# Performance work log

Hardware: AMD Instinct MI355X
Metric: run time of the kernel (lower is better)

## Reference

```python
import jax, jax.numpy as jnp
import numpy as np

B, T, D_IN, H, OUT = 512, 512, 64, 256, 64
EPS = 1e-5


def _ln(x, w, b):
    m = x.mean(-1, keepdims=True)
    v = ((x - m) ** 2).mean(-1, keepdims=True)
    return (x - m) / jnp.sqrt(v + EPS) * w + b


def _cell(x, h_prev, Wg, bg, gnw, gnb, Wc, bc, cnw, cnb):
    # LayerNormGRU cell
    combined = jnp.concatenate([x, h_prev], axis=-1)          # [B, D+H]
    rz = _ln(combined @ Wg.T + bg, gnw, gnb)                  # [B, 2H]
    r, z = jnp.split(rz, 2, axis=-1)
    r, z = jax.nn.sigmoid(r), jax.nn.sigmoid(z)
    combined_r = jnp.concatenate([x, r * h_prev], axis=-1)
    n = jnp.tanh(_ln(combined_r @ Wc.T + bc, cnw, cnb))       # [B, H]
    return (1.0 - z) * h_prev + z * n


def setup_inputs() -> dict:
    key = jax.random.key(0)
    ks = jax.random.split(key, 24)

    def uni(k, shape, fan_in):
        lim = 1.0 / np.sqrt(fan_in)
        return jax.random.uniform(k, shape, jnp.float32, -lim, lim)

    d0 = D_IN + H   # layer 0 cell input width
    d1 = H + H      # layer 1 cell input width
    return {
        "x": jax.random.normal(ks[0], (B, T, D_IN), jnp.float32),
        # layer 0
        "Wg0": uni(ks[1], (2 * H, d0), d0), "bg0": uni(ks[2], (2 * H,), d0),
        "gnw0": jnp.ones((2 * H,), jnp.float32), "gnb0": jnp.zeros((2 * H,), jnp.float32),
        "Wc0": uni(ks[3], (H, d0), d0), "bc0": uni(ks[4], (H,), d0),
        "cnw0": jnp.ones((H,), jnp.float32), "cnb0": jnp.zeros((H,), jnp.float32),
        # layer 1
        "Wg1": uni(ks[5], (2 * H, d1), d1), "bg1": uni(ks[6], (2 * H,), d1),
        "gnw1": jnp.ones((2 * H,), jnp.float32), "gnb1": jnp.zeros((2 * H,), jnp.float32),
        "Wc1": uni(ks[7], (H, d1), d1), "bc1": uni(ks[8], (H,), d1),
        "cnw1": jnp.ones((H,), jnp.float32), "cnb1": jnp.zeros((H,), jnp.float32),
        # output head
        "fcW": uni(ks[9], (OUT, H), H), "fcb": uni(ks[10], (OUT,), H),
    }


def reference(x, Wg0, bg0, gnw0, gnb0, Wc0, bc0, cnw0, cnb0,
              Wg1, bg1, gnw1, gnb1, Wc1, bc1, cnw1, cnb1, fcW, fcb):
    b = x.shape[0]
    h_init = (jnp.zeros((b, H), x.dtype), jnp.zeros((b, H), x.dtype))

    def step(carry, xt):
        h0, h1 = carry
        h0 = _cell(xt, h0, Wg0, bg0, gnw0, gnb0, Wc0, bc0, cnw0, cnb0)
        h1 = _cell(h0, h1, Wg1, bg1, gnw1, gnb1, Wc1, bc1, cnw1, cnb1)
        return (h0, h1), None

    (h0, h1), _ = jax.lax.scan(step, h_init, jnp.swapaxes(x, 0, 1))  # scan over T
    return h1 @ fcW.T + fcb  # [B, OUT]
```

## Files before the change

kernel.cpp:

```cpp
#include <hip/hip_runtime.h>


#define B_   512
#define T_   512
#define DIN  64
#define H_   256
#define OUT_ 64
#define EPS_ 1e-5f

typedef __attribute__((ext_vector_type(8))) short bf16x8;
typedef __attribute__((ext_vector_type(4))) float f32x4;

__device__ __forceinline__ unsigned short f2bf(float f) {
  unsigned int u = __float_as_uint(f);
  u += 0x7fffu + ((u >> 16) & 1u);
  return (unsigned short)(u >> 16);
}
__device__ __forceinline__ float bfh(unsigned short u) {
  return __uint_as_float(((unsigned int)u) << 16);
}
__device__ __forceinline__ float sigm_(float x) {
  return __builtin_amdgcn_rcpf(1.f + __expf(-x));
}
__device__ __forceinline__ float tanh_(float x) {
  return 1.f - 2.f * __builtin_amdgcn_rcpf(__expf(2.f * x) + 1.f);
}
template<int C>
__device__ __forceinline__ float dpp_add(float v) {
  int r = __builtin_amdgcn_update_dpp(0, __float_as_int(v), C, 0xF, 0xF, false);
  return v + __int_as_float(r);
}
__device__ __forceinline__ float red16(float v) {
  v = dpp_add<0x121>(v);
  v = dpp_add<0x122>(v);
  v = dpp_add<0x124>(v);
  v = dpp_add<0x128>(v);
  return v;
}

#define PIN8A(a) asm volatile("" : "+a"(a[0]), "+a"(a[1]), "+a"(a[2]), "+a"(a[3]), \
                                   "+a"(a[4]), "+a"(a[5]), "+a"(a[6]), "+a"(a[7]))

__global__ void prep_frag(const float* __restrict__ w, unsigned short* __restrict__ dst,
                          int N, int Ksrc, int koff) {
  int gid = blockIdx.x * 256 + threadIdx.x;
  if (gid >= N * 256) return;
  int n = gid >> 8, k = gid & 255;
  int idx = (((n >> 4) * 8 + (k >> 5)) * 64 + ((n & 15) + 16 * ((k >> 3) & 3))) * 8 + (k & 7);
  dst[idx] = f2bf(w[(size_t)n * Ksrc + koff + k]);
}

__global__ void prep_wx(const float* __restrict__ wg, const float* __restrict__ wc,
                        unsigned short* __restrict__ dst, int KX, int Kg, int Kc) {
  int gid = blockIdx.x * 256 + threadIdx.x;
  if (gid >= 768 * KX) return;
  int n = gid / KX, k = gid - n * KX;
  float v = (n < 512) ? wg[(size_t)n * Kg + k] : wc[(size_t)(n - 512) * Kc + k];
  dst[gid] = f2bf(v);
}

__global__ void bias_cat(const float* __restrict__ bg, const float* __restrict__ bc,
                         float* __restrict__ dst) {
  int i = blockIdx.x * 256 + threadIdx.x;
  if (i < 768) dst[i] = (i < 512) ? bg[i] : bc[i - 512];
}

__device__ __forceinline__ void precomp_tile(
    const void* __restrict__ Asrc, const unsigned short* __restrict__ wx,
    const float* __restrict__ bias, unsigned short* __restrict__ Pc,
    int TC, int t0, int KX, int AFP32,
    int mi, int nb, unsigned short* A_s, unsigned short* B_s, int t256)
{
  const int lane = t256 & 63, wv = t256 >> 6;
  const int m0 = mi * 128;
  const int bt = m0 / (TC * 16);
  const int tt0 = (m0 - bt * TC * 16) >> 4;
  const int mq = wv >> 1, nq = wv & 1;
  const int crow0 = (lane >> 4) * 4;

  f32x4 acc[4][4];
#pragma unroll
  for (int i = 0; i < 4; ++i)
#pragma unroll
    for (int j = 0; j < 4; ++j) acc[i][j] = (f32x4){0, 0, 0, 0};

  for (int kb = 0; kb < (KX >> 6); ++kb) {
    __syncthreads();
#pragma unroll
    for (int it = 0; it < 4; ++it) {
      int s = t256 + it * 256;
      int rg = s >> 3, k8 = s & 7;
      int mt = rg >> 4, r15 = rg & 15;
      int dl = r15 + 16 * (k8 & 3), kc = k8 >> 2;
      if (AFP32) {
        const float* xp = (const float*)Asrc +
            (((size_t)(bt * 16 + r15)) * T_ + (t0 + tt0 + mt)) * DIN + kb * 64 + k8 * 8;
        float4 u0 = *(const float4*)xp, u1 = *(const float4*)(xp + 4);
        unsigned short tmp[8];
        tmp[0] = f2bf(u0.x); tmp[1] = f2bf(u0.y); tmp[2] = f2bf(u0.z); tmp[3] = f2bf(u0.w);
        tmp[4] = f2bf(u1.x); tmp[5] = f2bf(u1.y); tmp[6] = f2bf(u1.z); tmp[7] = f2bf(u1.w);
        *reinterpret_cast<bf16x8*>(&A_s[((mt * 2 + kc) * 64 + dl) * 8]) =
            *reinterpret_cast<bf16x8*>(tmp);
      } else {
        const unsigned short* ap = (const unsigned short*)Asrc +
            ((size_t)(m0 + rg)) * KX + kb * 64 + k8 * 8;
        *reinterpret_cast<bf16x8*>(&A_s[((mt * 2 + kc) * 64 + dl) * 8]) =
            *reinterpret_cast<const bf16x8*>(ap);
      }
      const unsigned short* bp = wx + ((size_t)(nb + rg)) * KX + kb * 64 + k8 * 8;
      *reinterpret_cast<bf16x8*>(&B_s[((mt * 2 + kc) * 64 + dl) * 8]) =
          *reinterpret_cast<const bf16x8*>(bp);
    }
    __syncthreads();
#pragma unroll
    for (int kc = 0; kc < 2; ++kc) {
      bf16x8 av[4], bv[4];
#pragma unroll
      for (int i = 0; i < 4; ++i) {
        av[i] = *reinterpret_cast<const bf16x8*>(&A_s[(((mq * 4 + i) * 2 + kc) * 64 + lane) * 8]);
        bv[i] = *reinterpret_cast<const bf16x8*>(&B_s[(((nq * 4 + i) * 2 + kc) * 64 + lane) * 8]);
      }
#pragma unroll
      for (int i = 0; i < 4; ++i)
#pragma unroll
        for (int j = 0; j < 4; ++j)
          acc[i][j] = __builtin_amdgcn_mfma_f32_16x16x32_bf16(av[i], bv[j], acc[i][j], 0, 0, 0);
    }
  }
  float bb[4];
#pragma unroll
  for (int j = 0; j < 4; ++j) bb[j] = bias[nb + nq * 64 + j * 16 + (lane & 15)];
#pragma unroll
  for (int i = 0; i < 4; ++i) {
    int tt = tt0 + mq * 4 + i;
#pragma unroll
    for (int j = 0; j < 4; ++j) {
      int n = nb + nq * 64 + j * 16 + (lane & 15);
      ushort4 o;
      o.x = f2bf(acc[i][j][0] + bb[j]); o.y = f2bf(acc[i][j][1] + bb[j]);
      o.z = f2bf(acc[i][j][2] + bb[j]); o.w = f2bf(acc[i][j][3] + bb[j]);
      *reinterpret_cast<ushort4*>(&Pc[((size_t)(bt * TC + tt) * 768 + n) * 16 + crow0]) = o;
    }
  }
}

__launch_bounds__(256)
__global__ void precomp_std(const void* __restrict__ Asrc,
                            const unsigned short* __restrict__ wx,
                            const float* __restrict__ bias,
                            unsigned short* __restrict__ Pc,
                            int TC, int t0, int KX, int AFP32) {
  __shared__ __align__(16) unsigned short A_s[8192];
  __shared__ __align__(16) unsigned short B_s[8192];
  precomp_tile(Asrc, wx, bias, Pc, TC, t0, KX, AFP32,
               blockIdx.x, blockIdx.y * 128, A_s, B_s, threadIdx.x);
}

__device__ __forceinline__ void gru_body(
    unsigned char* smem, int bt,
    const unsigned short* __restrict__ gfrag,
    const unsigned short* __restrict__ cfrag,
    const unsigned short* __restrict__ Pc,
    const float* __restrict__ gnw, const float* __restrict__ gnb,
    const float* __restrict__ cnw, const float* __restrict__ cnb,
    float* __restrict__ hstate, unsigned short* __restrict__ h0out,
    int TC, int first)
{
  unsigned short* wc_s = (unsigned short*)smem;
  unsigned short (*h_s)[264]  = (unsigned short(*)[264])(smem + 131072);
  unsigned short (*rh_s)[264] = (unsigned short(*)[264])(smem + 139520);
  float (*sumP)[20] = (float(*)[20])(smem + 147968);
  float (*sqP)[20]  = (float(*)[20])(smem + 148608);

  const int tid = threadIdx.x, lane = tid & 63, wv = tid >> 6;
  const int b0 = bt * 16;
  const int arow = lane & 15, koff = (lane >> 4) * 8, crow0 = (lane >> 4) * 4;
  const int colr0 = 32 * wv + (lane & 15), colr1 = colr0 + 16;
  const int nt0 = 2 * wv, nt1 = 2 * wv + 1, nt2 = 16 + 2 * wv, nt3 = 17 + 2 * wv;

  for (int i = tid; i < 8192; i += 512)
    *reinterpret_cast<bf16x8*>(&wc_s[i * 8]) = *reinterpret_cast<const bf16x8*>(&cfrag[i * 8]);

  bf16x8 wgr0[8], wgr1[8], wgr2[8], wgr3[8];
#pragma unroll
  for (int kc = 0; kc < 8; ++kc) {
    wgr0[kc] = *reinterpret_cast<const bf16x8*>(&gfrag[((nt0 * 8 + kc) * 64 + lane) * 8]);
    wgr1[kc] = *reinterpret_cast<const bf16x8*>(&gfrag[((nt1 * 8 + kc) * 64 + lane) * 8]);
    wgr2[kc] = *reinterpret_cast<const bf16x8*>(&gfrag[((nt2 * 8 + kc) * 64 + lane) * 8]);
    wgr3[kc] = *reinterpret_cast<const bf16x8*>(&gfrag[((nt3 * 8 + kc) * 64 + lane) * 8]);
  }

  const float gw_r0 = gnw[colr0], gb_r0 = gnb[colr0];
  const float gw_r1 = gnw[colr1], gb_r1 = gnb[colr1];
  const float gw_z0 = gnw[256 + colr0], gb_z0 = gnb[256 + colr0];
  const float gw_z1 = gnw[256 + colr1], gb_z1 = gnb[256 + colr1];
  const float cw0 = cnw[colr0], cb0 = cnb[colr0];
  const float cw1 = cnw[colr1], cb1 = cnb[colr1];

  float hm[2][4];
  if (first) {
#pragma unroll
    for (int g = 0; g < 4; ++g) { hm[0][g] = 0.f; hm[1][g] = 0.f; }
    for (int i = tid; i < 16 * 264; i += 512) (&h_s[0][0])[i] = 0;
  } else {
#pragma unroll
    for (int g = 0; g < 4; ++g) {
      hm[0][g] = hstate[(size_t)(b0 + crow0 + g) * 256 + colr0];
      hm[1][g] = hstate[(size_t)(b0 + crow0 + g) * 256 + colr1];
    }
    int r = tid >> 5, c8 = (tid & 31) * 8;
    float4 v0 = *reinterpret_cast<const float4*>(&hstate[(size_t)(b0 + r) * 256 + c8]);
    float4 v1 = *reinterpret_cast<const float4*>(&hstate[(size_t)(b0 + r) * 256 + c8 + 4]);
    ushort4 o0, o1;
    o0.x = f2bf(v0.x); o0.y = f2bf(v0.y); o0.z = f2bf(v0.z); o0.w = f2bf(v0.w);
    o1.x = f2bf(v1.x); o1.y = f2bf(v1.y); o1.z = f2bf(v1.z); o1.w = f2bf(v1.w);
    *reinterpret_cast<ushort4*>(&h_s[r][c8]) = o0;
    *reinterpret_cast<ushort4*>(&h_s[r][c8 + 4]) = o1;
  }
  __syncthreads();

  const unsigned short* Pr = Pc + ((size_t)bt * TC * 768 + colr0) * 16;
  ushort4 npr0 = *reinterpret_cast<const ushort4*>(Pr + crow0);
  ushort4 npr1 = *reinterpret_cast<const ushort4*>(Pr + 256 + crow0);
  ushort4 npz0 = *reinterpret_cast<const ushort4*>(Pr + 4096 + crow0);
  ushort4 npz1 = *reinterpret_cast<const ushort4*>(Pr + 4352 + crow0);
  ushort4 npn0 = *reinterpret_cast<const ushort4*>(Pr + 8192 + crow0);
  ushort4 npn1 = *reinterpret_cast<const ushort4*>(Pr + 8448 + crow0);

  for (int tt = 0; tt < TC; ++tt) {
    PIN8A(wgr0); PIN8A(wgr1); PIN8A(wgr2); PIN8A(wgr3);

    ushort4 pr0 = npr0, pr1 = npr1, pz0 = npz0, pz1 = npz1, pn0 = npn0, pn1 = npn1;
    if (tt + 1 < TC) {
      Pr += 12288;
      npr0 = *reinterpret_cast<const ushort4*>(Pr + crow0);
      npr1 = *reinterpret_cast<const ushort4*>(Pr + 256 + crow0);
      npz0 = *reinterpret_cast<const ushort4*>(Pr + 4096 + crow0);
      npz1 = *reinterpret_cast<const ushort4*>(Pr + 4352 + crow0);
      npn0 = *reinterpret_cast<const ushort4*>(Pr + 8192 + crow0);
      npn1 = *reinterpret_cast<const ushort4*>(Pr + 8448 + crow0);
    }

    f32x4 a0 = {0, 0, 0, 0}, a1 = {0, 0, 0, 0}, a2 = {0, 0, 0, 0}, a3 = {0, 0, 0, 0};
#pragma unroll
    for (int kc = 0; kc < 8; ++kc) {
      bf16x8 av = *reinterpret_cast<const bf16x8*>(&h_s[arow][kc * 32 + koff]);
      a0 = __builtin_amdgcn_mfma_f32_16x16x32_bf16(av, wgr0[kc], a0, 0, 0, 0);
      a1 = __builtin_amdgcn_mfma_f32_16x16x32_bf16(av, wgr1[kc], a1, 0, 0, 0);
      a2 = __builtin_amdgcn_mfma_f32_16x16x32_bf16(av, wgr2[kc], a2, 0, 0, 0);
      a3 = __builtin_amdgcn_mfma_f32_16x16x32_bf16(av, wgr3[kc], a3, 0, 0, 0);
    }
    float vr0[4], vr1[4], vz0[4], vz1[4];
    {
      float s4[4], q4[4];
#pragma unroll
      for (int g = 0; g < 4; ++g) {
        vr0[g] = a0[g] + bfh(((const unsigned short*)&pr0)[g]);
        vr1[g] = a1[g] + bfh(((const unsigned short*)&pr1)[g]);
        vz0[g] = a2[g] + bfh(((const unsigned short*)&pz0)[g]);
        vz1[g] = a3[g] + bfh(((const unsigned short*)&pz1)[g]);
        s4[g] = red16(vr0[g] + vr1[g] + vz0[g] + vz1[g]);
        q4[g] = red16(vr0[g] * vr0[g] + vr1[g] * vr1[g] + vz0[g] * vz0[g] + vz1[g] * vz1[g]);
      }
      if ((lane & 15) == 0) {
        *reinterpret_cast<f32x4*>(&sumP[wv][crow0]) = (f32x4){s4[0], s4[1], s4[2], s4[3]};
        *reinterpret_cast<f32x4*>(&sqP[wv][crow0])  = (f32x4){q4[0], q4[1], q4[2], q4[3]};
      }
    }
    __syncthreads();

    float zf[2][4];
    {
      int sg = lane >> 4, rr = lane & 15;
      float S = sumP[2 * sg][rr] + sumP[2 * sg + 1][rr];
      float Q = sqP[2 * sg][rr] + sqP[2 * sg + 1][rr];
      S += __shfl_xor(S, 16, 64); Q += __shfl_xor(Q, 16, 64);
      S += __shfl_xor(S, 32, 64); Q += __shfl_xor(Q, 32, 64);
      float mn = S * (1.f / 512.f);
      float rs = __builtin_amdgcn_rsqf(Q * (1.f / 512.f) - mn * mn + EPS_);
#pragma unroll
      for (int g = 0; g < 4; ++g) {
        float m_ = __shfl(mn, crow0 + g, 64);
        float r_ = __shfl(rs, crow0 + g, 64);
        float rv0 = sigm_(fmaf((vr0[g] - m_) * r_, gw_r0, gb_r0));
        float rv1 = sigm_(fmaf((vr1[g] - m_) * r_, gw_r1, gb_r1));
        zf[0][g]  = sigm_(fmaf((vz0[g] - m_) * r_, gw_z0, gb_z0));
        zf[1][g]  = sigm_(fmaf((vz1[g] - m_) * r_, gw_z1, gb_z1));
        rh_s[crow0 + g][colr0] = f2bf(rv0 * hm[0][g]);
        rh_s[crow0 + g][colr1] = f2bf(rv1 * hm[1][g]);
      }
    }
    __syncthreads();

    f32x4 c0a = {0, 0, 0, 0}, c1a = {0, 0, 0, 0};
#pragma unroll
    for (int kc = 0; kc < 8; ++kc) {
      bf16x8 av = *reinterpret_cast<const bf16x8*>(&rh_s[arow][kc * 32 + koff]);
      bf16x8 b0v = *reinterpret_cast<const bf16x8*>(&wc_s[((nt0 * 8 + kc) * 64 + lane) * 8]);
      bf16x8 b1v = *reinterpret_cast<const bf16x8*>(&wc_s[((nt1 * 8 + kc) * 64 + lane) * 8]);
      c0a = __builtin_amdgcn_mfma_f32_16x16x32_bf16(av, b0v, c0a, 0, 0, 0);
      c1a = __builtin_amdgcn_mfma_f32_16x16x32_bf16(av, b1v, c1a, 0, 0, 0);
    }
    float vc0[4], vc1[4];
    {
      float s4[4], q4[4];
#pragma unroll
      for (int g = 0; g < 4; ++g) {
        vc0[g] = c0a[g] + bfh(((const unsigned short*)&pn0)[g]);
        vc1[g] = c1a[g] + bfh(((const unsigned short*)&pn1)[g]);
        s4[g] = red16(vc0[g] + vc1[g]);
        q4[g] = red16(vc0[g] * vc0[g] + vc1[g] * vc1[g]);
      }
      if ((lane & 15) == 0) {
        *reinterpret_cast<f32x4*>(&sumP[wv][crow0]) = (f32x4){s4[0], s4[1], s4[2], s4[3]};
        *reinterpret_cast<f32x4*>(&sqP[wv][crow0])  = (f32x4){q4[0], q4[1], q4[2], q4[3]};
      }
    }
    __syncthreads();

    {
      int sg = lane >> 4, rr = lane & 15;
      float S = sumP[2 * sg][rr] + sumP[2 * sg + 1][rr];
      float Q = sqP[2 * sg][rr] + sqP[2 * sg + 1][rr];
      S += __shfl_xor(S, 16, 64); Q += __shfl_xor(Q, 16, 64);
      S += __shfl_xor(S, 32, 64); Q += __shfl_xor(Q, 32, 64);
      float mn = S * (1.f / 256.f);
      float rs = __builtin_amdgcn_rsqf(Q * (1.f / 256.f) - mn * mn + EPS_);
      unsigned short* hrow = h0out ? (h0out + (size_t)(bt * TC + tt) * 4096) : (unsigned short*)nullptr;
#pragma unroll
      for (int g = 0; g < 4; ++g) {
        float m_ = __shfl(mn, crow0 + g, 64);
        float r_ = __shfl(rs, crow0 + g, 64);
        float n0 = tanh_(fmaf((vc0[g] - m_) * r_, cw0, cb0));
        float n1 = tanh_(fmaf((vc1[g] - m_) * r_, cw1, cb1));
        float h0n = fmaf(zf[0][g], n0 - hm[0][g], hm[0][g]);
        float h1n = fmaf(zf[1][g], n1 - hm[1][g], hm[1][g]);
        hm[0][g] = h0n; hm[1][g] = h1n;
        unsigned short hb0 = f2bf(h0n), hb1 = f2bf(h1n);
        h_s[crow0 + g][colr0] = hb0;
        h_s[crow0 + g][colr1] = hb1;
        if (hrow) {
          hrow[(size_t)(crow0 + g) * 256 + colr0] = hb0;
          hrow[(size_t)(crow0 + g) * 256 + colr1] = hb1;
        }
      }
    }
    __syncthreads();
  }

#pragma unroll
  for (int g = 0; g < 4; ++g) {
    hstate[(size_t)(b0 + crow0 + g) * 256 + colr0] = hm[0][g];
    hstate[(size_t)(b0 + crow0 + g) * 256 + colr1] = hm[1][g];
  }
}

__launch_bounds__(512, 2)
__global__ void mega(
    const float* __restrict__ x,
    const unsigned short* __restrict__ g0h, const unsigned short* __restrict__ c0h,
    const unsigned short* __restrict__ g1h, const unsigned short* __restrict__ c1h,
    const unsigned short* __restrict__ wx0, const unsigned short* __restrict__ wx1,
    const float* __restrict__ b768_0, const float* __restrict__ b768_1,
    const float* __restrict__ gnw0, const float* __restrict__ gnb0,
    const float* __restrict__ cnw0, const float* __restrict__ cnb0,
    const float* __restrict__ gnw1, const float* __restrict__ gnb1,
    const float* __restrict__ cnw1, const float* __restrict__ cnb1,
    float* __restrict__ hst0, float* __restrict__ hst1,
    unsigned short* __restrict__ P0a, unsigned short* __restrict__ P0b,
    unsigned short* __restrict__ P1a, unsigned short* __restrict__ P1b,
    unsigned short* __restrict__ h0a, unsigned short* __restrict__ h0b,
    int k, int TC, int NC)
{
  __shared__ __align__(16) unsigned char smem[149504];
  const int bid = blockIdx.x;

  if (bid < 32) {
    if (k >= NC) return;
    unsigned short* P0 = (k & 1) ? P0b : P0a;
    unsigned short* h0 = (k & 1) ? h0b : h0a;
    gru_body(smem, bid, g0h, c0h, P0, gnw0, gnb0, cnw0, cnb0, hst0, h0, TC, k == 0);
  } else if (bid < 64) {
    int kD = k - 2;
    if (kD < 0 || kD >= NC) return;
    unsigned short* P1 = (kD & 1) ? P1b : P1a;
    gru_body(smem, bid - 32, g1h, c1h, P1, gnw1, gnb1, cnw1, cnb1, hst1,
             (unsigned short*)nullptr, TC, kD == 0);
  } else if (bid < 160) {
    int kA = k + 1;
    if (kA >= NC) return;
    unsigned short* P0 = (kA & 1) ? P0b : P0a;
    int team = (bid - 64) * 2 + (threadIdx.x >> 8);
    int t256 = threadIdx.x & 255;
    unsigned short* A_s = (unsigned short*)(smem + (threadIdx.x >> 8) * 32768);
    unsigned short* B_s = A_s + 8192;
    int ntile = 24 * TC;
    for (int i = team; i < ntile; i += 192) {
      int mi = i % (4 * TC), ni = i / (4 * TC);
      precomp_tile(x, wx0, b768_0, P0, TC, kA * TC, 64, 1, mi, ni * 128, A_s, B_s, t256);
    }
  } else {
    int kC = k - 1;
    if (kC < 0 || kC >= NC) return;
    const unsigned short* h0 = (kC & 1) ? h0b : h0a;
    unsigned short* P1 = (kC & 1) ? P1b : P1a;
    int team = (bid - 160) * 2 + (threadIdx.x >> 8);
    int t256 = threadIdx.x & 255;
    unsigned short* A_s = (unsigned short*)(smem + (threadIdx.x >> 8) * 32768);
    unsigned short* B_s = A_s + 8192;
    int ntile = 24 * TC;
    for (int i = team; i < ntile; i += 192) {
      int mi = i % (4 * TC), ni = i / (4 * TC);
      precomp_tile(h0, wx1, b768_1, P1, TC, 0, 256, 0, mi, ni * 128, A_s, B_s, t256);
    }
  }
}

__launch_bounds__(256)
__global__ void head_k(const float* __restrict__ h1, const float* __restrict__ fcW,
                       const float* __restrict__ fcb, float* __restrict__ out) {
  __shared__ float hs[16][256];
  const int tid = threadIdx.x, b0 = blockIdx.x * 16;
  for (int i = tid; i < 16 * 64; i += 256) {
    int r = i >> 6, c4 = (i & 63) * 4;
    *reinterpret_cast<float4*>(&hs[r][c4]) =
        *reinterpret_cast<const float4*>(&h1[(size_t)(b0 + r) * 256 + c4]);
  }
  __syncthreads();
  int r = tid >> 4, o = (tid & 15) * 4;
  float a0 = fcb[o], a1 = fcb[o + 1], a2 = fcb[o + 2], a3 = fcb[o + 3];
  for (int k = 0; k < 256; ++k) {
    float h = hs[r][k];
    a0 = fmaf(h, fcW[(size_t)(o + 0) * 256 + k], a0);
    a1 = fmaf(h, fcW[(size_t)(o + 1) * 256 + k], a1);
    a2 = fmaf(h, fcW[(size_t)(o + 2) * 256 + k], a2);
    a3 = fmaf(h, fcW[(size_t)(o + 3) * 256 + k], a3);
  }
  float4 ov = {a0, a1, a2, a3};
  *reinterpret_cast<float4*>(&out[(size_t)(b0 + r) * 64 + o]) = ov;
}

extern "C" void kernel_launch(void* const* d_in, const int* in_sizes, int n_in,
                              void* d_out, int out_size, void* d_ws, size_t ws_size,
                              hipStream_t stream) {
  (void)in_sizes; (void)n_in; (void)out_size;
  const float* x    = (const float*)d_in[0];
  const float* Wg0  = (const float*)d_in[1];
  const float* bg0  = (const float*)d_in[2];
  const float* gnw0 = (const float*)d_in[3];
  const float* gnb0 = (const float*)d_in[4];
  const float* Wc0  = (const float*)d_in[5];
  const float* bc0  = (const float*)d_in[6];
  const float* cnw0 = (const float*)d_in[7];
  const float* cnb0 = (const float*)d_in[8];
  const float* Wg1  = (const float*)d_in[9];
  const float* bg1  = (const float*)d_in[10];
  const float* gnw1 = (const float*)d_in[11];
  const float* gnb1 = (const float*)d_in[12];
  const float* Wc1  = (const float*)d_in[13];
  const float* bc1  = (const float*)d_in[14];
  const float* cnw1 = (const float*)d_in[15];
  const float* cnb1 = (const float*)d_in[16];
  const float* fcW  = (const float*)d_in[17];
  const float* fcb  = (const float*)d_in[18];

  float* hst0 = (float*)d_ws;
  float* hst1 = hst0 + 131072;
  float* b768_0 = hst1 + 131072;
  float* b768_1 = b768_0 + 768;
  unsigned short* g0h = (unsigned short*)(b768_1 + 768);
  unsigned short* c0h = g0h + 131072;
  unsigned short* g1h = c0h + 65536;
  unsigned short* c1h = g1h + 131072;
  unsigned short* wx0 = c1h + 65536;
  unsigned short* wx1 = wx0 + 49152;
  unsigned short* dynbase = wx1 + 196608;

  const size_t fixed_bytes = (size_t)((char*)dynbase - (char*)d_ws);
  int TC = 32;
  while (TC > 4) {
    size_t need = fixed_bytes + (size_t)TC * 3670016;
    if (need <= ws_size) break;
    TC >>= 1;
  }
  const int NC = T_ / TC;

  unsigned short* P0a = dynbase;
  unsigned short* P0b = P0a + (size_t)TC * 393216;
  unsigned short* P1a = P0b + (size_t)TC * 393216;
  unsigned short* P1b = P1a + (size_t)TC * 393216;
  unsigned short* h0a = P1b + (size_t)TC * 393216;
  unsigned short* h0b = h0a + (size_t)TC * 131072;

  prep_frag<<<512, 256, 0, stream>>>(Wg0, g0h, 512, 320, 64);
  prep_frag<<<256, 256, 0, stream>>>(Wc0, c0h, 256, 320, 64);
  prep_frag<<<512, 256, 0, stream>>>(Wg1, g1h, 512, 512, 256);
  prep_frag<<<256, 256, 0, stream>>>(Wc1, c1h, 256, 512, 256);
  prep_wx<<<192, 256, 0, stream>>>(Wg0, Wc0, wx0, 64, 320, 320);
  prep_wx<<<768, 256, 0, stream>>>(Wg1, Wc1, wx1, 256, 512, 512);
  bias_cat<<<3, 256, 0, stream>>>(bg0, bc0, b768_0);
  bias_cat<<<3, 256, 0, stream>>>(bg1, bc1, b768_1);

  precomp_std<<<dim3(4 * TC, 6), 256, 0, stream>>>(x, wx0, b768_0, P0a, TC, 0, 64, 1);

  for (int k = 0; k < NC + 2; ++k) {
    mega<<<256, 512, 0, stream>>>(x, g0h, c0h, g1h, c1h, wx0, wx1, b768_0, b768_1,
        gnw0, gnb0, cnw0, cnb0, gnw1, gnb1, cnw1, cnb1,
        hst0, hst1, P0a, P0b, P1a, P1b, h0a, h0b, k, TC, NC);
  }

  head_k<<<32, 256, 0, stream>>>(hst1, fcW, fcb, (float*)d_out);
}
```

Before: 2.630 ms.

## Interleave two batch tiles per GRU block to overlap recurrent phases

Each recurrent GRU block now handles two 16-row batch tiles (X and Y) and interleaves their gate/candidate phases, so one tile's matmul runs while the other's layernorm reduction is pending. This halves the number of recurrent blocks (16 per layer instead of 32) and gives the freed CUs to the input-projection precompute teams (stride 224 instead of 192). The aim is to hide barrier and reduction latency in the serial time loop. The cost is a longer per-step critical path per block, the removal of the P prefetch-ahead, and more shared memory per block.

```diff
diff --git a/kernel.cpp b/kernel.cpp
--- a/kernel.cpp
+++ b/kernel.cpp
@@ -156,8 +156,8 @@
                blockIdx.x, blockIdx.y * 128, A_s, B_s, threadIdx.x);
 }
 
-__device__ __forceinline__ void gru_body(
-    unsigned char* smem, int bt,
+__device__ __forceinline__ void gru_body2(
+    unsigned char* smem, int blk,
     const unsigned short* __restrict__ gfrag,
     const unsigned short* __restrict__ cfrag,
     const unsigned short* __restrict__ Pc,
@@ -167,13 +167,17 @@
     int TC, int first)
 {
   unsigned short* wc_s = (unsigned short*)smem;
-  unsigned short (*h_s)[264]  = (unsigned short(*)[264])(smem + 131072);
-  unsigned short (*rh_s)[264] = (unsigned short(*)[264])(smem + 139520);
-  float (*sumP)[20] = (float(*)[20])(smem + 147968);
-  float (*sqP)[20]  = (float(*)[20])(smem + 148608);
+  unsigned short (*h_sX)[264] = (unsigned short(*)[264])(smem + 131072);
+  unsigned short (*h_sY)[264] = (unsigned short(*)[264])(smem + 139520);
+  unsigned short (*rh_s)[264] = (unsigned short(*)[264])(smem + 147968);
+  float* sumX = (float*)(smem + 156416);
+  float* sqX  = (float*)(smem + 156928);
+  float* sumY = (float*)(smem + 157440);
+  float* sqY  = (float*)(smem + 157952);
 
   const int tid = threadIdx.x, lane = tid & 63, wv = tid >> 6;
-  const int b0 = bt * 16;
+  const int bt0 = 2 * blk, bt1 = 2 * blk + 1;
+  const int b0X = bt0 * 16, b0Y = bt1 * 16;
   const int arow = lane & 15, koff = (lane >> 4) * 8, crow0 = (lane >> 4) * 4;
   const int colr0 = 32 * wv + (lane & 15), colr1 = colr0 + 16;
   const int nt0 = 2 * wv, nt1 = 2 * wv + 1, nt2 = 16 + 2 * wv, nt3 = 17 + 2 * wv;
@@ -197,83 +201,106 @@
   const float cw0 = cnw[colr0], cb0 = cnb[colr0];
   const float cw1 = cnw[colr1], cb1 = cnb[colr1];
 
-  float hm[2][4];
+  float hmX[2][4], hmY[2][4];
   if (first) {
 #pragma unroll
-    for (int g = 0; g < 4; ++g) { hm[0][g] = 0.f; hm[1][g] = 0.f; }
-    for (int i = tid; i < 16 * 264; i += 512) (&h_s[0][0])[i] = 0;
+    for (int g = 0; g < 4; ++g) {
+      hmX[0][g] = 0.f; hmX[1][g] = 0.f; hmY[0][g] = 0.f; hmY[1][g] = 0.f;
+    }
+    for (int i = tid; i < 16 * 264; i += 512) {
+      (&h_sX[0][0])[i] = 0; (&h_sY[0][0])[i] = 0;
+    }
   } else {
 #pragma unroll
     for (int g = 0; g < 4; ++g) {
-      hm[0][g] = hstate[(size_t)(b0 + crow0 + g) * 256 + colr0];
-      hm[1][g] = hstate[(size_t)(b0 + crow0 + g) * 256 + colr1];
+      hmX[0][g] = hstate[(size_t)(b0X + crow0 + g) * 256 + colr0];
+      hmX[1][g] = hstate[(size_t)(b0X + crow0 + g) * 256 + colr1];
+      hmY[0][g] = hstate[(size_t)(b0Y + crow0 + g) * 256 + colr0];
+      hmY[1][g] = hstate[(size_t)(b0Y + crow0 + g) * 256 + colr1];
     }
     int r = tid >> 5, c8 = (tid & 31) * 8;
-    float4 v0 = *reinterpret_cast<const float4*>(&hstate[(size_t)(b0 + r) * 256 + c8]);
-    float4 v1 = *reinterpret_cast<const float4*>(&hstate[(size_t)(b0 + r) * 256 + c8 + 4]);
-    ushort4 o0, o1;
-    o0.x = f2bf(v0.x); o0.y = f2bf(v0.y); o0.z = f2bf(v0.z); o0.w = f2bf(v0.w);
-    o1.x = f2bf(v1.x); o1.y = f2bf(v1.y); o1.z = f2bf(v1.z); o1.w = f2bf(v1.w);
-    *reinterpret_cast<ushort4*>(&h_s[r][c8]) = o0;
-    *reinterpret_cast<ushort4*>(&h_s[r][c8 + 4]) = o1;
+    {
+      float4 v0 = *reinterpret_cast<const float4*>(&hstate[(size_t)(b0X + r) * 256 + c8]);
+      float4 v1 = *reinterpret_cast<const float4*>(&hstate[(size_t)(b0X + r) * 256 + c8 + 4]);
+      ushort4 o0, o1;
+      o0.x = f2bf(v0.x); o0.y = f2bf(v0.y); o0.z = f2bf(v0.z); o0.w = f2bf(v0.w);
+      o1.x = f2bf(v1.x); o1.y = f2bf(v1.y); o1.z = f2bf(v1.z); o1.w = f2bf(v1.w);
+      *reinterpret_cast<ushort4*>(&h_sX[r][c8]) = o0;
+      *reinterpret_cast<ushort4*>(&h_sX[r][c8 + 4]) = o1;
+    }
+    {
+      float4 v0 = *reinterpret_cast<const float4*>(&hstate[(size_t)(b0Y + r) * 256 + c8]);
+      float4 v1 = *reinterpret_cast<const float4*>(&hstate[(size_t)(b0Y + r) * 256 + c8 + 4]);
+      ushort4 o0, o1;
+      o0.x = f2bf(v0.x); o0.y = f2bf(v0.y); o0.z = f2bf(v0.z); o0.w = f2bf(v0.w);
+      o1.x = f2bf(v1.x); o1.y = f2bf(v1.y); o1.z = f2bf(v1.z); o1.w = f2bf(v1.w);
+      *reinterpret_cast<ushort4*>(&h_sY[r][c8]) = o0;
+      *reinterpret_cast<ushort4*>(&h_sY[r][c8 + 4]) = o1;
+    }
   }
   __syncthreads();
 
-  const unsigned short* Pr = Pc + ((size_t)bt * TC * 768 + colr0) * 16;
-  ushort4 npr0 = *reinterpret_cast<const ushort4*>(Pr + crow0);
-  ushort4 npr1 = *reinterpret_cast<const ushort4*>(Pr + 256 + crow0);
-  ushort4 npz0 = *reinterpret_cast<const ushort4*>(Pr + 4096 + crow0);
-  ushort4 npz1 = *reinterpret_cast<const ushort4*>(Pr + 4352 + crow0);
-  ushort4 npn0 = *reinterpret_cast<const ushort4*>(Pr + 8192 + crow0);
-  ushort4 npn1 = *reinterpret_cast<const ushort4*>(Pr + 8448 + crow0);
+  const unsigned short* PrX = Pc + ((size_t)bt0 * TC * 768 + colr0) * 16;
+  const unsigned short* PrY = Pc + ((size_t)bt1 * TC * 768 + colr0) * 16;
 
   for (int tt = 0; tt < TC; ++tt) {
     PIN8A(wgr0); PIN8A(wgr1); PIN8A(wgr2); PIN8A(wgr3);
 
-    ushort4 pr0 = npr0, pr1 = npr1, pz0 = npz0, pz1 = npz1, pn0 = npn0, pn1 = npn1;
-    if (tt + 1 < TC) {
-      Pr += 12288;
-      npr0 = *reinterpret_cast<const ushort4*>(Pr + crow0);
-      npr1 = *reinterpret_cast<const ushort4*>(Pr + 256 + crow0);
-      npz0 = *reinterpret_cast<const ushort4*>(Pr + 4096 + crow0);
-      npz1 = *reinterpret_cast<const ushort4*>(Pr + 4352 + crow0);
-      npn0 = *reinterpret_cast<const ushort4*>(Pr + 8192 + crow0);
-      npn1 = *reinterpret_cast<const ushort4*>(Pr + 8448 + crow0);
-    }
-
-    f32x4 a0 = {0, 0, 0, 0}, a1 = {0, 0, 0, 0}, a2 = {0, 0, 0, 0}, a3 = {0, 0, 0, 0};
+    ushort4 xr0 = *reinterpret_cast<const ushort4*>(PrX + crow0);
+    ushort4 xr1 = *reinterpret_cast<const ushort4*>(PrX + 256 + crow0);
+    ushort4 xz0 = *reinterpret_cast<const ushort4*>(PrX + 4096 + crow0);
+    ushort4 xz1 = *reinterpret_cast<const ushort4*>(PrX + 4352 + crow0);
+    f32x4 a0 = {0,0,0,0}, a1 = {0,0,0,0}, a2 = {0,0,0,0}, a3 = {0,0,0,0};
 #pragma unroll
     for (int kc = 0; kc < 8; ++kc) {
-      bf16x8 av = *reinterpret_cast<const bf16x8*>(&h_s[arow][kc * 32 + koff]);
+      bf16x8 av = *reinterpret_cast<const bf16x8*>(&h_sX[arow][kc * 32 + koff]);
       a0 = __builtin_amdgcn_mfma_f32_16x16x32_bf16(av, wgr0[kc], a0, 0, 0, 0);
       a1 = __builtin_amdgcn_mfma_f32_16x16x32_bf16(av, wgr1[kc], a1, 0, 0, 0);
       a2 = __builtin_amdgcn_mfma_f32_16x16x32_bf16(av, wgr2[kc], a2, 0, 0, 0);
       a3 = __builtin_amdgcn_mfma_f32_16x16x32_bf16(av, wgr3[kc], a3, 0, 0, 0);
     }
-    float vr0[4], vr1[4], vz0[4], vz1[4];
-    {
-      float s4[4], q4[4];
-#pragma unroll
-      for (int g = 0; g < 4; ++g) {
-        vr0[g] = a0[g] + bfh(((const unsigned short*)&pr0)[g]);
-        vr1[g] = a1[g] + bfh(((const unsigned short*)&pr1)[g]);
-        vz0[g] = a2[g] + bfh(((const unsigned short*)&pz0)[g]);
-        vz1[g] = a3[g] + bfh(((const unsigned short*)&pz1)[g]);
-        s4[g] = red16(vr0[g] + vr1[g] + vz0[g] + vz1[g]);
-        q4[g] = red16(vr0[g] * vr0[g] + vr1[g] * vr1[g] + vz0[g] * vz0[g] + vz1[g] * vz1[g]);
-      }
-      if ((lane & 15) == 0) {
-        *reinterpret_cast<f32x4*>(&sumP[wv][crow0]) = (f32x4){s4[0], s4[1], s4[2], s4[3]};
-        *reinterpret_cast<f32x4*>(&sqP[wv][crow0])  = (f32x4){q4[0], q4[1], q4[2], q4[3]};
-      }
+    float vrX0[4], vrX1[4], vzX0[4], vzX1[4];
+#pragma unroll
+    for (int g = 0; g < 4; ++g) {
+      vrX0[g] = a0[g] + bfh(((const unsigned short*)&xr0)[g]);
+      vrX1[g] = a1[g] + bfh(((const unsigned short*)&xr1)[g]);
+      vzX0[g] = a2[g] + bfh(((const unsigned short*)&xz0)[g]);
+      vzX1[g] = a3[g] + bfh(((const unsigned short*)&xz1)[g]);
+      float s = red16(vrX0[g] + vrX1[g] + vzX0[g] + vzX1[g]);
+      float q = red16(vrX0[g]*vrX0[g] + vrX1[g]*vrX1[g] + vzX0[g]*vzX0[g] + vzX1[g]*vzX1[g]);
+      if ((lane & 15) == 0) { sumX[wv * 16 + crow0 + g] = s; sqX[wv * 16 + crow0 + g] = q; }
     }
     __syncthreads();
 
-    float zf[2][4];
+    ushort4 yr0 = *reinterpret_cast<const ushort4*>(PrY + crow0);
+    ushort4 yr1 = *reinterpret_cast<const ushort4*>(PrY + 256 + crow0);
+    ushort4 yz0 = *reinterpret_cast<const ushort4*>(PrY + 4096 + crow0);
+    ushort4 yz1 = *reinterpret_cast<const ushort4*>(PrY + 4352 + crow0);
+    f32x4 b0 = {0,0,0,0}, b1 = {0,0,0,0}, b2 = {0,0,0,0}, b3 = {0,0,0,0};
+#pragma unroll
+    for (int kc = 0; kc < 8; ++kc) {
+      bf16x8 av = *reinterpret_cast<const bf16x8*>(&h_sY[arow][kc * 32 + koff]);
+      b0 = __builtin_amdgcn_mfma_f32_16x16x32_bf16(av, wgr0[kc], b0, 0, 0, 0);
+      b1 = __builtin_amdgcn_mfma_f32_16x16x32_bf16(av, wgr1[kc], b1, 0, 0, 0);
+      b2 = __builtin_amdgcn_mfma_f32_16x16x32_bf16(av, wgr2[kc], b2, 0, 0, 0);
+      b3 = __builtin_amdgcn_mfma_f32_16x16x32_bf16(av, wgr3[kc], b3, 0, 0, 0);
+    }
+    float vrY0[4], vrY1[4], vzY0[4], vzY1[4];
+#pragma unroll
+    for (int g = 0; g < 4; ++g) {
+      vrY0[g] = b0[g] + bfh(((const unsigned short*)&yr0)[g]);
+      vrY1[g] = b1[g] + bfh(((const unsigned short*)&yr1)[g]);
+      vzY0[g] = b2[g] + bfh(((const unsigned short*)&yz0)[g]);
+      vzY1[g] = b3[g] + bfh(((const unsigned short*)&yz1)[g]);
+      float s = red16(vrY0[g] + vrY1[g] + vzY0[g] + vzY1[g]);
+      float q = red16(vrY0[g]*vrY0[g] + vrY1[g]*vrY1[g] + vzY0[g]*vzY0[g] + vzY1[g]*vzY1[g]);
+      if ((lane & 15) == 0) { sumY[wv * 16 + crow0 + g] = s; sqY[wv * 16 + crow0 + g] = q; }
+    }
+    float zfX[2][4];
     {
       int sg = lane >> 4, rr = lane & 15;
-      float S = sumP[2 * sg][rr] + sumP[2 * sg + 1][rr];
-      float Q = sqP[2 * sg][rr] + sqP[2 * sg + 1][rr];
+      float S = sumX[2 * sg * 16 + rr] + sumX[(2 * sg + 1) * 16 + rr];
+      float Q = sqX[2 * sg * 16 + rr] + sqX[(2 * sg + 1) * 16 + rr];
       S += __shfl_xor(S, 16, 64); Q += __shfl_xor(Q, 16, 64);
       S += __shfl_xor(S, 32, 64); Q += __shfl_xor(Q, 32, 64);
       float mn = S * (1.f / 512.f);
@@ -282,63 +309,86 @@
       for (int g = 0; g < 4; ++g) {
         float m_ = __shfl(mn, crow0 + g, 64);
         float r_ = __shfl(rs, crow0 + g, 64);
-        float rv0 = sigm_(fmaf((vr0[g] - m_) * r_, gw_r0, gb_r0));
-        float rv1 = sigm_(fmaf((vr1[g] - m_) * r_, gw_r1, gb_r1));
-        zf[0][g]  = sigm_(fmaf((vz0[g] - m_) * r_, gw_z0, gb_z0));
-        zf[1][g]  = sigm_(fmaf((vz1[g] - m_) * r_, gw_z1, gb_z1));
-        rh_s[crow0 + g][colr0] = f2bf(rv0 * hm[0][g]);
-        rh_s[crow0 + g][colr1] = f2bf(rv1 * hm[1][g]);
+        float rv0 = sigm_(fmaf((vrX0[g] - m_) * r_, gw_r0, gb_r0));
+        float rv1 = sigm_(fmaf((vrX1[g] - m_) * r_, gw_r1, gb_r1));
+        zfX[0][g] = sigm_(fmaf((vzX0[g] - m_) * r_, gw_z0, gb_z0));
+        zfX[1][g] = sigm_(fmaf((vzX1[g] - m_) * r_, gw_z1, gb_z1));
+        rh_s[crow0 + g][colr0] = f2bf(rv0 * hmX[0][g]);
+        rh_s[crow0 + g][colr1] = f2bf(rv1 * hmX[1][g]);
       }
     }
     __syncthreads();
 
-    f32x4 c0a = {0, 0, 0, 0}, c1a = {0, 0, 0, 0};
+    ushort4 xn0 = *reinterpret_cast<const ushort4*>(PrX + 8192 + crow0);
+    ushort4 xn1 = *reinterpret_cast<const ushort4*>(PrX + 8448 + crow0);
+    f32x4 c0 = {0,0,0,0}, c1 = {0,0,0,0};
 #pragma unroll
     for (int kc = 0; kc < 8; ++kc) {
       bf16x8 av = *reinterpret_cast<const bf16x8*>(&rh_s[arow][kc * 32 + koff]);
-      bf16x8 b0v = *reinterpret_cast<const bf16x8*>(&wc_s[((nt0 * 8 + kc) * 64 + lane) * 8]);
-      bf16x8 b1v = *reinterpret_cast<const bf16x8*>(&wc_s[((nt1 * 8 + kc) * 64 + lane) * 8]);
-      c0a = __builtin_amdgcn_mfma_f32_16x16x32_bf16(av, b0v, c0a, 0, 0, 0);
-      c1a = __builtin_amdgcn_mfma_f32_16x16x32_bf16(av, b1v, c1a, 0, 0, 0);
-    }
-    float vc0[4], vc1[4];
-    {
-      float s4[4], q4[4];
-#pragma unroll
-      for (int g = 0; g < 4; ++g) {
-        vc0[g] = c0a[g] + bfh(((const unsigned short*)&pn0)[g]);
-        vc1[g] = c1a[g] + bfh(((const unsigned short*)&pn1)[g]);
-        s4[g] = red16(vc0[g] + vc1[g]);
-        q4[g] = red16(vc0[g] * vc0[g] + vc1[g] * vc1[g]);
-      }
-      if ((lane & 15) == 0) {
-        *reinterpret_cast<f32x4*>(&sumP[wv][crow0]) = (f32x4){s4[0], s4[1], s4[2], s4[3]};
-        *reinterpret_cast<f32x4*>(&sqP[wv][crow0])  = (f32x4){q4[0], q4[1], q4[2], q4[3]};
-      }
-    }
-    __syncthreads();
-
+      bf16x8 w0 = *reinterpret_cast<const bf16x8*>(&wc_s[((nt0 * 8 + kc) * 64 + lane) * 8]);
+      bf16x8 w1 = *reinterpret_cast<const bf16x8*>(&wc_s[((nt1 * 8 + kc) * 64 + lane) * 8]);
+      c0 = __builtin_amdgcn_mfma_f32_16x16x32_bf16(av, w0, c0, 0, 0, 0);
+      c1 = __builtin_amdgcn_mfma_f32_16x16x32_bf16(av, w1, c1, 0, 0, 0);
+    }
+    float vcX0[4], vcX1[4];
+#pragma unroll
+    for (int g = 0; g < 4; ++g) {
+      vcX0[g] = c0[g] + bfh(((const unsigned short*)&xn0)[g]);
+      vcX1[g] = c1[g] + bfh(((const unsigned short*)&xn1)[g]);
+      float s = red16(vcX0[g] + vcX1[g]);
+      float q = red16(vcX0[g]*vcX0[g] + vcX1[g]*vcX1[g]);
+      if ((lane & 15) == 0) { sumX[wv * 16 + crow0 + g] = s; sqX[wv * 16 + crow0 + g] = q; }
+    }
+    float zfY[2][4], rhv0[4], rhv1[4];
     {
       int sg = lane >> 4, rr = lane & 15;
-      float S = sumP[2 * sg][rr] + sumP[2 * sg + 1][rr];
-      float Q = sqP[2 * sg][rr] + sqP[2 * sg + 1][rr];
+      float S = sumY[2 * sg * 16 + rr] + sumY[(2 * sg + 1) * 16 + rr];
+      float Q = sqY[2 * sg * 16 + rr] + sqY[(2 * sg + 1) * 16 + rr];
+      S += __shfl_xor(S, 16, 64); Q += __shfl_xor(Q, 16, 64);
+      S += __shfl_xor(S, 32, 64); Q += __shfl_xor(Q, 32, 64);
+      float mn = S * (1.f / 512.f);
+      float rs = __builtin_amdgcn_rsqf(Q * (1.f / 512.f) - mn * mn + EPS_);
+#pragma unroll
+      for (int g = 0; g < 4; ++g) {
+        float m_ = __shfl(mn, crow0 + g, 64);
+        float r_ = __shfl(rs, crow0 + g, 64);
+        float rv0 = sigm_(fmaf((vrY0[g] - m_) * r_, gw_r0, gb_r0));
+        float rv1 = sigm_(fmaf((vrY1[g] - m_) * r_, gw_r1, gb_r1));
+        zfY[0][g] = sigm_(fmaf((vzY0[g] - m_) * r_, gw_z0, gb_z0));
+        zfY[1][g] = sigm_(fmaf((vzY1[g] - m_) * r_, gw_z1, gb_z1));
+        rhv0[g] = rv0 * hmY[0][g];
+        rhv1[g] = rv1 * hmY[1][g];
+      }
+    }
+    __syncthreads();
+
+#pragma unroll
+    for (int g = 0; g < 4; ++g) {
+      rh_s[crow0 + g][colr0] = f2bf(rhv0[g]);
+      rh_s[crow0 + g][colr1] = f2bf(rhv1[g]);
+    }
+    {
+      int sg = lane >> 4, rr = lane & 15;
+      float S = sumX[2 * sg * 16 + rr] + sumX[(2 * sg + 1) * 16 + rr];
+      float Q = sqX[2 * sg * 16 + rr] + sqX[(2 * sg + 1) * 16 + rr];
       S += __shfl_xor(S, 16, 64); Q += __shfl_xor(Q, 16, 64);
       S += __shfl_xor(S, 32, 64); Q += __shfl_xor(Q, 32, 64);
       float mn = S * (1.f / 256.f);
       float rs = __builtin_amdgcn_rsqf(Q * (1.f / 256.f) - mn * mn + EPS_);
-      unsigned short* hrow = h0out ? (h0out + (size_t)(bt * TC + tt) * 4096) : (unsigned short*)nullptr;
+      unsigned short* hrow = h0out ? (h0out + (size_t)(bt0 * TC + tt) * 4096)
+                                   : (unsigned short*)nullptr;
 #pragma unroll
       for (int g = 0; g < 4; ++g) {
         float m_ = __shfl(mn, crow0 + g, 64);
         float r_ = __shfl(rs, crow0 + g, 64);
-        float n0 = tanh_(fmaf((vc0[g] - m_) * r_, cw0, cb0));
-        float n1 = tanh_(fmaf((vc1[g] - m_) * r_, cw1, cb1));
-        float h0n = fmaf(zf[0][g], n0 - hm[0][g], hm[0][g]);
-        float h1n = fmaf(zf[1][g], n1 - hm[1][g], hm[1][g]);
-        hm[0][g] = h0n; hm[1][g] = h1n;
+        float n0 = tanh_(fmaf((vcX0[g] - m_) * r_, cw0, cb0));
+        float n1 = tanh_(fmaf((vcX1[g] - m_) * r_, cw1, cb1));
+        float h0n = fmaf(zfX[0][g], n0 - hmX[0][g], hmX[0][g]);
+        float h1n = fmaf(zfX[1][g], n1 - hmX[1][g], hmX[1][g]);
+        hmX[0][g] = h0n; hmX[1][g] = h1n;
         unsigned short hb0 = f2bf(h0n), hb1 = f2bf(h1n);
-        h_s[crow0 + g][colr0] = hb0;
-        h_s[crow0 + g][colr1] = hb1;
+        h_sX[crow0 + g][colr0] = hb0;
+        h_sX[crow0 + g][colr1] = hb1;
         if (hrow) {
           hrow[(size_t)(crow0 + g) * 256 + colr0] = hb0;
           hrow[(size_t)(crow0 + g) * 256 + colr1] = hb1;
@@ -346,12 +396,67 @@
       }
     }
     __syncthreads();
-  }
+
+    ushort4 yn0 = *reinterpret_cast<const ushort4*>(PrY + 8192 + crow0);
+    ushort4 yn1 = *reinterpret_cast<const ushort4*>(PrY + 8448 + crow0);
+    f32x4 d0 = {0,0,0,0}, d1 = {0,0,0,0};
+#pragma unroll
+    for (int kc = 0; kc < 8; ++kc) {
+      bf16x8 av = *reinterpret_cast<const bf16x8*>(&rh_s[arow][kc * 32 + koff]);
+      bf16x8 w0 = *reinterpret_cast<const bf16x8*>(&wc_s[((nt0 * 8 + kc) * 64 + lane) * 8]);
+      bf16x8 w1 = *reinterpret_cast<const bf16x8*>(&wc_s[((nt1 * 8 + kc) * 64 + lane) * 8]);
+      d0 = __builtin_amdgcn_mfma_f32_16x16x32_bf16(av, w0, d0, 0, 0, 0);
+      d1 = __builtin_amdgcn_mfma_f32_16x16x32_bf16(av, w1, d1, 0, 0, 0);
+    }
+    float vcY0[4], vcY1[4];
+#pragma unroll
+    for (int g = 0; g < 4; ++g) {
+      vcY0[g] = d0[g] + bfh(((const unsigned short*)&yn0)[g]);
+      vcY1[g] = d1[g] + bfh(((const unsigned short*)&yn1)[g]);
+      float s = red16(vcY0[g] + vcY1[g]);
+      float q = red16(vcY0[g]*vcY0[g] + vcY1[g]*vcY1[g]);
+      if ((lane & 15) == 0) { sumY[wv * 16 + crow0 + g] = s; sqY[wv * 16 + crow0 + g] = q; }
+    }
+    __syncthreads();
+
+    {
+      int sg = lane >> 4, rr = lane & 15;
+      float S = sumY[2 * sg * 16 + rr] + sumY[(2 * sg + 1) * 16 + rr];
+      float Q = sqY[2 * sg * 16 + rr] + sqY[(2 * sg + 1) * 16 + rr];
+      S += __shfl_xor(S, 16, 64); Q += __shfl_xor(Q, 16, 64);
+      S += __shfl_xor(S, 32, 64); Q += __shfl_xor(Q, 32, 64);
+      float mn = S * (1.f / 256.f);
+      float rs = __builtin_amdgcn_rsqf(Q * (1.f / 256.f) - mn * mn + EPS_);
+      unsigned short* hrow = h0out ? (h0out + (size_t)(bt1 * TC + tt) * 4096)
+                                   : (unsigned short*)nullptr;
+#pragma unroll
+      for (int g = 0; g < 4; ++g) {
+        float m_ = __shfl(mn, crow0 + g, 64);
+        float r_ = __shfl(rs, crow0 + g, 64);
+        float n0 = tanh_(fmaf((vcY0[g] - m_) * r_, cw0, cb0));
+        float n1 = tanh_(fmaf((vcY1[g] - m_) * r_, cw1, cb1));
+        float h0n = fmaf(zfY[0][g], n0 - hmY[0][g], hmY[0][g]);
+        float h1n = fmaf(zfY[1][g], n1 - hmY[1][g], hmY[1][g]);
+        hmY[0][g] = h0n; hmY[1][g] = h1n;
+        unsigned short hb0 = f2bf(h0n), hb1 = f2bf(h1n);
+        h_sY[crow0 + g][colr0] = hb0;
+        h_sY[crow0 + g][colr1] = hb1;
+        if (hrow) {
+          hrow[(size_t)(crow0 + g) * 256 + colr0] = hb0;
+          hrow[(size_t)(crow0 + g) * 256 + colr1] = hb1;
+        }
+      }
+    }
+    PrX += 12288; PrY += 12288;
+  }
+  __syncthreads();
 
 #pragma unroll
   for (int g = 0; g < 4; ++g) {
-    hstate[(size_t)(b0 + crow0 + g) * 256 + colr0] = hm[0][g];
-    hstate[(size_t)(b0 + crow0 + g) * 256 + colr1] = hm[1][g];
+    hstate[(size_t)(b0X + crow0 + g) * 256 + colr0] = hmX[0][g];
+    hstate[(size_t)(b0X + crow0 + g) * 256 + colr1] = hmX[1][g];
+    hstate[(size_t)(b0Y + crow0 + g) * 256 + colr0] = hmY[0][g];
+    hstate[(size_t)(b0Y + crow0 + g) * 256 + colr1] = hmY[1][g];
   }
 }
 
@@ -372,30 +477,30 @@
     unsigned short* __restrict__ h0a, unsigned short* __restrict__ h0b,
     int k, int TC, int NC)
 {
-  __shared__ __align__(16) unsigned char smem[149504];
+  __shared__ __align__(16) unsigned char smem[158976];
   const int bid = blockIdx.x;
 
-  if (bid < 32) {
+  if (bid < 16) {
     if (k >= NC) return;
     unsigned short* P0 = (k & 1) ? P0b : P0a;
     unsigned short* h0 = (k & 1) ? h0b : h0a;
-    gru_body(smem, bid, g0h, c0h, P0, gnw0, gnb0, cnw0, cnb0, hst0, h0, TC, k == 0);
-  } else if (bid < 64) {
+    gru_body2(smem, bid, g0h, c0h, P0, gnw0, gnb0, cnw0, cnb0, hst0, h0, TC, k == 0);
+  } else if (bid < 32) {
     int kD = k - 2;
     if (kD < 0 || kD >= NC) return;
     unsigned short* P1 = (kD & 1) ? P1b : P1a;
-    gru_body(smem, bid - 32, g1h, c1h, P1, gnw1, gnb1, cnw1, cnb1, hst1,
-             (unsigned short*)nullptr, TC, kD == 0);
-  } else if (bid < 160) {
+    gru_body2(smem, bid - 16, g1h, c1h, P1, gnw1, gnb1, cnw1, cnb1, hst1,
+              (unsigned short*)nullptr, TC, kD == 0);
+  } else if (bid < 144) {
     int kA = k + 1;
     if (kA >= NC) return;
     unsigned short* P0 = (kA & 1) ? P0b : P0a;
-    int team = (bid - 64) * 2 + (threadIdx.x >> 8);
+    int team = (bid - 32) * 2 + (threadIdx.x >> 8);
     int t256 = threadIdx.x & 255;
     unsigned short* A_s = (unsigned short*)(smem + (threadIdx.x >> 8) * 32768);
     unsigned short* B_s = A_s + 8192;
     int ntile = 24 * TC;
-    for (int i = team; i < ntile; i += 192) {
+    for (int i = team; i < ntile; i += 224) {
       int mi = i % (4 * TC), ni = i / (4 * TC);
       precomp_tile(x, wx0, b768_0, P0, TC, kA * TC, 64, 1, mi, ni * 128, A_s, B_s, t256);
     }
@@ -404,12 +509,12 @@
     if (kC < 0 || kC >= NC) return;
     const unsigned short* h0 = (kC & 1) ? h0b : h0a;
     unsigned short* P1 = (kC & 1) ? P1b : P1a;
-    int team = (bid - 160) * 2 + (threadIdx.x >> 8);
+    int team = (bid - 144) * 2 + (threadIdx.x >> 8);
     int t256 = threadIdx.x & 255;
     unsigned short* A_s = (unsigned short*)(smem + (threadIdx.x >> 8) * 32768);
     unsigned short* B_s = A_s + 8192;
     int ntile = 24 * TC;
-    for (int i = team; i < ntile; i += 192) {
+    for (int i = team; i < ntile; i += 224) {
       int mi = i % (4 * TC), ni = i / (4 * TC);
       precomp_tile(h0, wx1, b768_1, P1, TC, 0, 256, 0, mi, ni * 128, A_s, B_s, t256);
     }
```

Result: slower. 8.112 ms (+208.5%).
